# Performance work log

Hardware: AMD Instinct MI355X
Metric: run time of the kernel (lower is better)

The kernel has to match this reference:

```python
import jax, jax.numpy as jnp
import numpy as np

N = 50000      # num_nodes
SEQ = 52       # seq_len (weeks)
FIN = 16       # in_channels
H = 128        # hidden_dim
E = 800000     # num edges (before self-loops)
NEG_SLOPE = 0.2


def setup_inputs() -> dict:
    key = jax.random.key(0)
    ks = jax.random.split(key, 10)
    return {
        "x_seq": jax.random.normal(ks[0], (SEQ, N, FIN), jnp.float32),
        "edge_index": jax.random.randint(ks[1], (2, E), 0, N),
        "Wg": jax.random.normal(ks[2], (FIN, H), jnp.float32) * 0.1,       # GAT linear (no bias on lin in PyG default path; bias added at end)
        "att_src": jax.random.normal(ks[3], (H,), jnp.float32) * 0.1,
        "att_dst": jax.random.normal(ks[4], (H,), jnp.float32) * 0.1,
        "bias_g": jnp.zeros((H,), jnp.float32),
        "W_ih": jax.random.normal(ks[5], (3 * H, H), jnp.float32) * 0.05,  # GRUCell input weights (r,z,n order)
        "W_hh": jax.random.normal(ks[6], (3 * H, H), jnp.float32) * 0.05,
        "b_ih": jnp.zeros((3 * H,), jnp.float32),
        "b_hh": jnp.zeros((3 * H,), jnp.float32),
        "W_fc": jax.random.normal(ks[7], (1, H), jnp.float32) * 0.1,
        "b_fc": jnp.zeros((1,), jnp.float32),
    }


def _gat(x, src, dst, Wg, att_src, att_dst, bias_g):
    # x: [N, FIN] -> xp: [N, H]
    xp = x @ Wg
    a_s = xp @ att_src  # [N]
    a_d = xp @ att_dst  # [N]
    e = jax.nn.leaky_relu(a_s[src] + a_d[dst], NEG_SLOPE)          # [E+N] edge scores
    m = jax.ops.segment_max(e, dst, num_segments=N)                # softmax over incoming edges per dst
    w = jnp.exp(e - m[dst])
    denom = jax.ops.segment_sum(w, dst, num_segments=N)
    alpha = w / denom[dst]
    out = jax.ops.segment_sum(alpha[:, None] * xp[src], dst, num_segments=N)  # [N, H]
    return out + bias_g


def _gru_cell(x, h, W_ih, W_hh, b_ih, b_hh):
    gi = x @ W_ih.T + b_ih  # [N, 3H]
    gh = h @ W_hh.T + b_hh
    i_r, i_z, i_n = jnp.split(gi, 3, axis=1)
    h_r, h_z, h_n = jnp.split(gh, 3, axis=1)
    r = jax.nn.sigmoid(i_r + h_r)
    z = jax.nn.sigmoid(i_z + h_z)
    n = jnp.tanh(i_n + r * h_n)
    return (1.0 - z) * n + z * h


def reference(x_seq, edge_index, Wg, att_src, att_dst, bias_g, W_ih, W_hh, b_ih, b_hh, W_fc, b_fc):
    # PyG GATConv add_self_loops=True
    loop = jnp.arange(N)
    src = jnp.concatenate([edge_index[0], loop])
    dst = jnp.concatenate([edge_index[1], loop])

    def step(h, xt):
        spatial = jax.nn.relu(_gat(xt, src, dst, Wg, att_src, att_dst, bias_g))
        h_new = _gru_cell(spatial, h, W_ih, W_hh, b_ih, b_hh)
        return h_new, None

    h0 = jnp.zeros((N, H), jnp.float32)
    hT, _ = jax.lax.scan(step, h0, x_seq)
    return hT @ W_fc.T + b_fc  # [N, 1]
```

## Files before the change

kernel.cpp:

```cpp
#include <hip/hip_runtime.h>
#include <math.h>

#define NN 50000
#define SEQ 52
#define FIN 16
#define HD 128
#define NEG_SLOPE 0.2f

typedef short bf16x8 __attribute__((ext_vector_type(8)));
typedef float f32x16 __attribute__((ext_vector_type(16)));

__device__ __forceinline__ short f2bf(float x) {
    unsigned u = __float_as_uint(x);
    u += 0x7fffu + ((u >> 16) & 1u);
    return (short)(u >> 16);
}
__device__ __forceinline__ float b2f(short s) {
    return __uint_as_float(((unsigned)(unsigned short)s) << 16);
}

__global__ void deg_init_kernel(int* deg, int n) {
    int i = blockIdx.x * blockDim.x + threadIdx.x;
    if (i < n) deg[i] = 1;
}

__global__ void deg_count_kernel(const int* __restrict__ dst, int* deg, int e) {
    int i = blockIdx.x * blockDim.x + threadIdx.x;
    if (i < e) atomicAdd(&deg[dst[i]], 1);
}

__global__ __launch_bounds__(1024) void scan_kernel(const int* __restrict__ deg,
                                                    int* row_ptr, int n) {
    __shared__ int buf[1024];
    __shared__ int carry;
    int tid = threadIdx.x;
    if (tid == 0) carry = 0;
    __syncthreads();
    for (int base = 0; base < n; base += 1024) {
        int i = base + tid;
        int v = (i < n) ? deg[i] : 0;
        buf[tid] = v;
        __syncthreads();
        for (int off = 1; off < 1024; off <<= 1) {
            int t = (tid >= off) ? buf[tid - off] : 0;
            __syncthreads();
            buf[tid] += t;
            __syncthreads();
        }
        if (i < n) row_ptr[i] = carry + buf[tid] - v;
        __syncthreads();
        if (tid == 1023) carry += buf[1023];
        __syncthreads();
    }
    if (tid == 0) row_ptr[n] = carry;
}

__global__ void selfloop_kernel(const int* __restrict__ row_ptr, int* cursor,
                                int* col, int n) {
    int i = blockIdx.x * blockDim.x + threadIdx.x;
    if (i < n) {
        int p = row_ptr[i];
        col[p] = i;
        cursor[i] = p + 1;
    }
}

__global__ void scatter_kernel(const int* __restrict__ src, const int* __restrict__ dst,
                               int* cursor, int* col, int e) {
    int i = blockIdx.x * blockDim.x + threadIdx.x;
    if (i < e) {
        int p = atomicAdd(&cursor[dst[i]], 1);
        col[p] = src[i];
    }
}

__global__ void wpack_kernel(const float* __restrict__ Wi, const float* __restrict__ Wh,
                             short* __restrict__ wfrag) {
    int idx = blockIdx.x * blockDim.x + threadIdx.x;
    if (idx >= 3 * 4 * 8 * 4 * 64) return;
    int lane = idx & 63;
    int which = (idx >> 6) & 3;
    int ks = (idx >> 8) & 7;
    int slab = (idx >> 11) & 3;
    int g = idx >> 13;
    int col = slab * 32 + (lane & 31);
    int kcol = ks * 16 + (lane >> 5) * 8;
    const float* Wsrc = (which < 2) ? Wi : Wh;
    const float* row = Wsrc + (size_t)(g * HD + col) * HD + kcol;
    short* dstp = wfrag + (size_t)idx * 8;
    bool lo = (which & 1);
#pragma unroll
    for (int e = 0; e < 8; ++e) {
        float v = row[e];
        short hi = f2bf(v);
        dstp[e] = lo ? f2bf(v - b2f(hi)) : hi;
    }
}


__global__ __launch_bounds__(256) void xp_kernel(
    const float* __restrict__ x, const float* __restrict__ Wg,
    const float* __restrict__ att_src, const float* __restrict__ att_dst,
    unsigned* __restrict__ xpb, float* __restrict__ a_s, float* __restrict__ a_d, int n) {
    int wave = (blockIdx.x * blockDim.x + threadIdx.x) >> 6;
    int lane = threadIdx.x & 63;
    if (wave >= n) return;
    const float* xr = x + (size_t)wave * FIN;
    float xv[FIN];
#pragma unroll
    for (int k = 0; k < FIN; ++k) xv[k] = xr[k];
    int c0 = 2 * lane, c1 = 2 * lane + 1;
    float v0 = 0.f, v1 = 0.f;
#pragma unroll
    for (int k = 0; k < FIN; ++k) {
        v0 += xv[k] * Wg[k * HD + c0];
        v1 += xv[k] * Wg[k * HD + c1];
    }
    unsigned p = (unsigned)(unsigned short)f2bf(v0) |
                 ((unsigned)(unsigned short)f2bf(v1) << 16);
    xpb[(size_t)wave * 64 + lane] = p;
    float s = v0 * att_src[c0] + v1 * att_src[c1];
    float d = v0 * att_dst[c0] + v1 * att_dst[c1];
#pragma unroll
    for (int off = 32; off; off >>= 1) {
        s += __shfl_xor(s, off);
        d += __shfl_xor(d, off);
    }
    if (lane == 0) { a_s[wave] = s; a_d[wave] = d; }
}

__global__ __launch_bounds__(256) void gat_kernel(
    const int* __restrict__ row_ptr, const int* __restrict__ col,
    const float* __restrict__ a_s, const float* __restrict__ a_d,
    const short* __restrict__ xpb, const float* __restrict__ bias_g,
    float* __restrict__ spatial, int n) {
    int wave = (blockIdx.x * blockDim.x + threadIdx.x) >> 6;
    int lane = threadIdx.x & 63;
    if (wave >= n) return;
    int start = row_ptr[wave], end = row_ptr[wave + 1];
    int eg = lane >> 4;
    int fg = lane & 15;
    float ad = a_d[wave];
    float acc[8] = {0.f, 0.f, 0.f, 0.f, 0.f, 0.f, 0.f, 0.f};
    float dpart = 0.f;

    for (int base = start; base < end; base += 64) {
        int cnt = end - base;
        if (cnt > 64) cnt = 64;

        int s = 0;
        float wgt = 0.f;
        if (lane < cnt) {
            s = col[base + lane];
            float e = a_s[s] + ad;
            e = (e > 0.f) ? e : NEG_SLOPE * e;
            wgt = __expf(e);
        }
        dpart += wgt;

        int nk = (cnt + 3) >> 2;
        int k = 0;
        for (; k + 2 <= nk; k += 2) {
            int e0 = eg + 4 * k;
            int e1 = e0 + 4;
            int c0 = (e0 < cnt) ? e0 : 0;
            int c1 = (e1 < cnt) ? e1 : 0;
            int si0 = __shfl(s, c0);
            int si1 = __shfl(s, c1);
            float w0 = __shfl(wgt, c0);
            float w1 = __shfl(wgt, c1);
            if (e0 >= cnt) w0 = 0.f;
            if (e1 >= cnt) w1 = 0.f;
            bf16x8 r0 = *(const bf16x8*)(xpb + (size_t)si0 * HD + fg * 8);
            bf16x8 r1 = *(const bf16x8*)(xpb + (size_t)si1 * HD + fg * 8);
#pragma unroll
            for (int j = 0; j < 8; ++j) acc[j] += w0 * b2f(r0[j]);
#pragma unroll
            for (int j = 0; j < 8; ++j) acc[j] += w1 * b2f(r1[j]);
        }
        if (k < nk) {
            int e0 = eg + 4 * k;
            int c0 = (e0 < cnt) ? e0 : 0;
            int si0 = __shfl(s, c0);
            float w0 = __shfl(wgt, c0);
            if (e0 >= cnt) w0 = 0.f;
            bf16x8 r0 = *(const bf16x8*)(xpb + (size_t)si0 * HD + fg * 8);
#pragma unroll
            for (int j = 0; j < 8; ++j) acc[j] += w0 * b2f(r0[j]);
        }
    }

#pragma unroll
    for (int off = 32; off; off >>= 1) dpart += __shfl_xor(dpart, off);
#pragma unroll
    for (int j = 0; j < 8; ++j) {
        acc[j] += __shfl_xor(acc[j], 16);
        acc[j] += __shfl_xor(acc[j], 32);
    }
    float inv = 1.f / dpart;
#pragma unroll
    for (int jj = 0; jj < 2; ++jj) {
        int f = fg * 8 + eg * 2 + jj;
        float o = acc[eg * 2 + jj] * inv + bias_g[f];
        spatial[(size_t)wave * HD + f] = fmaxf(o, 0.f);
    }
}

__global__ __launch_bounds__(256, 2) void gru_mfma_kernel(
    const float* __restrict__ spatial, float* __restrict__ h,
    const short* __restrict__ wfrag,
    const float* __restrict__ b_ih, const float* __restrict__ b_hh, int n) {
    __shared__ bf16x8 sSH[512];
    __shared__ bf16x8 sSL[512];
    __shared__ bf16x8 sHH[512];
    __shared__ bf16x8 sHL[512];

    int t = threadIdx.x;
    int lane = t & 63;
    int w = t >> 6;
    int n0 = blockIdx.x * 32;

#pragma unroll
    for (int q = 0; q < 2; ++q) {
        int ks = w * 2 + q;
        int row = n0 + (lane & 31);
        if (row >= n) row = n - 1;
        int kcol = ks * 16 + (lane >> 5) * 8;
        const float* sp = spatial + (size_t)row * HD + kcol;
        const float* hp = h + (size_t)row * HD + kcol;
        float s8[8], h8[8];
        *(float4*)(s8) = *(const float4*)(sp);
        *(float4*)(s8 + 4) = *(const float4*)(sp + 4);
        *(float4*)(h8) = *(const float4*)(hp);
        *(float4*)(h8 + 4) = *(const float4*)(hp + 4);
        bf16x8 sh, sl, hh, hl;
#pragma unroll
        for (int j = 0; j < 8; ++j) {
            short a = f2bf(s8[j]);
            sh[j] = a;
            sl[j] = f2bf(s8[j] - b2f(a));
            short b = f2bf(h8[j]);
            hh[j] = b;
            hl[j] = f2bf(h8[j] - b2f(b));
        }
        int li = ks * 64 + lane;
        sSH[li] = sh; sSL[li] = sl; sHH[li] = hh; sHL[li] = hl;
    }
    __syncthreads();

    int j0 = w * 32;
    int cj = lane & 31;
    int kh = lane >> 5;

    f32x16 arz[2], ain, ahn;
#pragma unroll
    for (int r = 0; r < 16; ++r) {
        arz[0][r] = 0.f; arz[1][r] = 0.f; ain[r] = 0.f; ahn[r] = 0.f;
    }

    const short* wb = wfrag + (size_t)w * 16384 + (size_t)lane * 8;

    bf16x8 wv[3][12];
#pragma unroll
    for (int p = 0; p < 2; ++p) {
#pragma unroll
        for (int g = 0; g < 3; ++g) {
#pragma unroll
            for (int q = 0; q < 4; ++q)
                wv[p][g * 4 + q] = *(const bf16x8*)(wb + g * 65536 + p * 2048 + q * 512);
        }
    }

#pragma unroll
    for (int ks = 0; ks < 8; ++ks) {
        int cur = ks % 3;
        if (ks < 6) {
            int nxt = (ks + 2) % 3;
#pragma unroll
            for (int g = 0; g < 3; ++g) {
#pragma unroll
                for (int q = 0; q < 4; ++q)
                    wv[nxt][g * 4 + q] =
                        *(const bf16x8*)(wb + g * 65536 + (ks + 2) * 2048 + q * 512);
            }
        }
        int li = ks * 64 + lane;
        bf16x8 aSH = sSH[li];
        bf16x8 aSL = sSL[li];
        bf16x8 aHH = sHH[li];
        bf16x8 aHL = sHL[li];
#pragma unroll
        for (int g = 0; g < 2; ++g) {
            bf16x8 wih = wv[cur][g * 4 + 0];
            bf16x8 wil = wv[cur][g * 4 + 1];
            bf16x8 whh = wv[cur][g * 4 + 2];
            bf16x8 whl = wv[cur][g * 4 + 3];
            arz[g] = __builtin_amdgcn_mfma_f32_32x32x16_bf16(aSH, wih, arz[g], 0, 0, 0);
            arz[g] = __builtin_amdgcn_mfma_f32_32x32x16_bf16(aHH, whh, arz[g], 0, 0, 0);
            arz[g] = __builtin_amdgcn_mfma_f32_32x32x16_bf16(aSL, wih, arz[g], 0, 0, 0);
            arz[g] = __builtin_amdgcn_mfma_f32_32x32x16_bf16(aHL, whh, arz[g], 0, 0, 0);
            arz[g] = __builtin_amdgcn_mfma_f32_32x32x16_bf16(aSH, wil, arz[g], 0, 0, 0);
            arz[g] = __builtin_amdgcn_mfma_f32_32x32x16_bf16(aHH, whl, arz[g], 0, 0, 0);
        }
        {
            bf16x8 wih = wv[cur][8];
            bf16x8 wil = wv[cur][9];
            bf16x8 whh = wv[cur][10];
            bf16x8 whl = wv[cur][11];
            ain = __builtin_amdgcn_mfma_f32_32x32x16_bf16(aSH, wih, ain, 0, 0, 0);
            ahn = __builtin_amdgcn_mfma_f32_32x32x16_bf16(aHH, whh, ahn, 0, 0, 0);
            ain = __builtin_amdgcn_mfma_f32_32x32x16_bf16(aSL, wih, ain, 0, 0, 0);
            ahn = __builtin_amdgcn_mfma_f32_32x32x16_bf16(aHL, whh, ahn, 0, 0, 0);
            ain = __builtin_amdgcn_mfma_f32_32x32x16_bf16(aSH, wil, ain, 0, 0, 0);
            ahn = __builtin_amdgcn_mfma_f32_32x32x16_bf16(aHH, whl, ahn, 0, 0, 0);
        }
    }

    int j = j0 + cj;
    float brz0 = b_ih[j] + b_hh[j];
    float brz1 = b_ih[HD + j] + b_hh[HD + j];
    float bin_ = b_ih[2 * HD + j];
    float bhn = b_hh[2 * HD + j];
    const short* hhs = (const short*)sHH;
    const short* hls = (const short*)sHL;
    int ksj = j >> 4, halfj = (j >> 3) & 1, ej = j & 7;

#pragma unroll
    for (int r = 0; r < 16; ++r) {
        int nl = (r & 3) + 8 * (r >> 2) + 4 * kh;
        int node = n0 + nl;
        if (node < n) {
            float rr = 1.f / (1.f + __expf(-(arz[0][r] + brz0)));
            float zz = 1.f / (1.f + __expf(-(arz[1][r] + brz1)));
            float nn2 = tanhf(ain[r] + bin_ + rr * (ahn[r] + bhn));
            int li = (ksj * 64 + nl + 32 * halfj) * 8 + ej;
            float hold = b2f(hhs[li]) + b2f(hls[li]);
            h[(size_t)node * HD + j] = (1.f - zz) * nn2 + zz * hold;
        }
    }
}

__global__ __launch_bounds__(256) void fc_kernel(
    const float* __restrict__ h, const float* __restrict__ W_fc,
    const float* __restrict__ b_fc, float* __restrict__ out, int n) {
    int wave = (blockIdx.x * blockDim.x + threadIdx.x) >> 6;
    int lane = threadIdx.x & 63;
    if (wave >= n) return;
    float v = h[(size_t)wave * HD + lane] * W_fc[lane] +
              h[(size_t)wave * HD + lane + 64] * W_fc[lane + 64];
#pragma unroll
    for (int off = 32; off; off >>= 1) v += __shfl_xor(v, off);
    if (lane == 0) out[wave] = v + b_fc[0];
}

extern "C" void kernel_launch(void* const* d_in, const int* in_sizes, int n_in,
                              void* d_out, int out_size, void* d_ws, size_t ws_size,
                              hipStream_t stream) {
    const float* x_seq   = (const float*)d_in[0];
    const int*   ei      = (const int*)d_in[1];
    const float* Wg      = (const float*)d_in[2];
    const float* att_src = (const float*)d_in[3];
    const float* att_dst = (const float*)d_in[4];
    const float* bias_g  = (const float*)d_in[5];
    const float* W_ih    = (const float*)d_in[6];
    const float* W_hh    = (const float*)d_in[7];
    const float* b_ih    = (const float*)d_in[8];
    const float* b_hh    = (const float*)d_in[9];
    const float* W_fc    = (const float*)d_in[10];
    const float* b_fc    = (const float*)d_in[11];
    float* out = (float*)d_out;

    const int N = NN;
    const int E = in_sizes[1] / 2;
    const int* src = ei;
    const int* dst = ei + E;

    char* w = (char*)d_ws;
    size_t off = 0;
    auto alloc = [&](size_t bytes) {
        char* p = w + off;
        off = (off + bytes + 255) & ~(size_t)255;
        return p;
    };
    int*   deg     = (int*)alloc((size_t)N * 4);
    int*   row_ptr = (int*)alloc((size_t)(N + 1) * 4);
    int*   cursor  = (int*)alloc((size_t)N * 4);
    int*   col     = (int*)alloc((size_t)(E + N) * 4);
    float* a_s     = (float*)alloc((size_t)N * 4);
    float* a_d     = (float*)alloc((size_t)N * 4);
    unsigned* xpb  = (unsigned*)alloc((size_t)N * 64 * 4);
    float* spatial = (float*)alloc((size_t)N * HD * 4);
    float* hbuf    = (float*)alloc((size_t)N * HD * 4);
    short* wfrag   = (short*)alloc((size_t)3 * 4 * 8 * 4 * 64 * 8 * 2);

    hipMemsetAsync(hbuf, 0, (size_t)N * HD * 4, stream);

    deg_init_kernel<<<(N + 255) / 256, 256, 0, stream>>>(deg, N);
    deg_count_kernel<<<(E + 255) / 256, 256, 0, stream>>>(dst, deg, E);
    scan_kernel<<<1, 1024, 0, stream>>>(deg, row_ptr, N);
    selfloop_kernel<<<(N + 255) / 256, 256, 0, stream>>>(row_ptr, cursor, col, N);
    scatter_kernel<<<(E + 255) / 256, 256, 0, stream>>>(src, dst, cursor, col, E);
    wpack_kernel<<<(24576 + 255) / 256, 256, 0, stream>>>(W_ih, W_hh, wfrag);

    int node_wave_blocks = (N * 64 + 255) / 256;
    int gru_blocks = (N + 31) / 32;

    for (int t = 0; t < SEQ; ++t) {
        const float* xt = x_seq + (size_t)t * N * FIN;
        xp_kernel<<<node_wave_blocks, 256, 0, stream>>>(xt, Wg, att_src, att_dst,
                                                        xpb, a_s, a_d, N);
        gat_kernel<<<node_wave_blocks, 256, 0, stream>>>(row_ptr, col, a_s, a_d,
                                                         (const short*)xpb, bias_g,
                                                         spatial, N);
        gru_mfma_kernel<<<gru_blocks, 256, 0, stream>>>(spatial, hbuf, wfrag,
                                                        b_ih, b_hh, N);
    }
    fc_kernel<<<node_wave_blocks, 256, 0, stream>>>(hbuf, W_fc, b_fc, out, N);
}
```

Measured before the change: 6.574 ms.

## Process two node tiles per GRU block and unroll GAT gather by four

The GRU MFMA kernel now covers 64 nodes per block in two 32-row tiles, so each loaded weight fragment feeds both tiles. This halves the weight traffic per node, but it drops the register prefetch pipeline for weights and doubles the accumulators and shared memory. The GAT aggregation loop is unrolled to four edges per iteration so more gather loads are in flight at once. Division, sigmoid and tanh are replaced by fast __fdividef/__expf forms, which trade a little accuracy for fewer instructions.

```diff
diff --git a/kernel.cpp b/kernel.cpp
--- a/kernel.cpp
+++ b/kernel.cpp
@@ -160,25 +160,27 @@
 
         int nk = (cnt + 3) >> 2;
         int k = 0;
-        for (; k + 2 <= nk; k += 2) {
-            int e0 = eg + 4 * k;
-            int e1 = e0 + 4;
-            int c0 = (e0 < cnt) ? e0 : 0;
-            int c1 = (e1 < cnt) ? e1 : 0;
-            int si0 = __shfl(s, c0);
-            int si1 = __shfl(s, c1);
-            float w0 = __shfl(wgt, c0);
-            float w1 = __shfl(wgt, c1);
-            if (e0 >= cnt) w0 = 0.f;
-            if (e1 >= cnt) w1 = 0.f;
-            bf16x8 r0 = *(const bf16x8*)(xpb + (size_t)si0 * HD + fg * 8);
-            bf16x8 r1 = *(const bf16x8*)(xpb + (size_t)si1 * HD + fg * 8);
-#pragma unroll
-            for (int j = 0; j < 8; ++j) acc[j] += w0 * b2f(r0[j]);
-#pragma unroll
-            for (int j = 0; j < 8; ++j) acc[j] += w1 * b2f(r1[j]);
-        }
-        if (k < nk) {
+        for (; k + 4 <= nk; k += 4) {
+            int si[4];
+            float wt[4];
+#pragma unroll
+            for (int u = 0; u < 4; ++u) {
+                int e0 = eg + 4 * (k + u);
+                int c0 = (e0 < cnt) ? e0 : 0;
+                si[u] = __shfl(s, c0);
+                wt[u] = __shfl(wgt, c0);
+                if (e0 >= cnt) wt[u] = 0.f;
+            }
+            bf16x8 r[4];
+#pragma unroll
+            for (int u = 0; u < 4; ++u)
+                r[u] = *(const bf16x8*)(xpb + (size_t)si[u] * HD + fg * 8);
+#pragma unroll
+            for (int u = 0; u < 4; ++u)
+#pragma unroll
+                for (int j = 0; j < 8; ++j) acc[j] += wt[u] * b2f(r[u][j]);
+        }
+        for (; k < nk; ++k) {
             int e0 = eg + 4 * k;
             int c0 = (e0 < cnt) ? e0 : 0;
             int si0 = __shfl(s, c0);
@@ -197,7 +199,7 @@
         acc[j] += __shfl_xor(acc[j], 16);
         acc[j] += __shfl_xor(acc[j], 32);
     }
-    float inv = 1.f / dpart;
+    float inv = __fdividef(1.f, dpart);
 #pragma unroll
     for (int jj = 0; jj < 2; ++jj) {
         int f = fg * 8 + eg * 2 + jj;
@@ -210,20 +212,21 @@
     const float* __restrict__ spatial, float* __restrict__ h,
     const short* __restrict__ wfrag,
     const float* __restrict__ b_ih, const float* __restrict__ b_hh, int n) {
-    __shared__ bf16x8 sSH[512];
-    __shared__ bf16x8 sSL[512];
-    __shared__ bf16x8 sHH[512];
-    __shared__ bf16x8 sHL[512];
+    __shared__ bf16x8 sSH[2][512];
+    __shared__ bf16x8 sSL[2][512];
+    __shared__ bf16x8 sHH[2][512];
+    __shared__ bf16x8 sHL[2][512];
 
     int t = threadIdx.x;
     int lane = t & 63;
     int w = t >> 6;
-    int n0 = blockIdx.x * 32;
-
-#pragma unroll
-    for (int q = 0; q < 2; ++q) {
-        int ks = w * 2 + q;
-        int row = n0 + (lane & 31);
+    int n0 = blockIdx.x * 64;
+
+#pragma unroll
+    for (int q = 0; q < 4; ++q) {
+        int tile = q >> 1;
+        int ks = w * 2 + (q & 1);
+        int row = n0 + tile * 32 + (lane & 31);
         if (row >= n) row = n - 1;
         int kcol = ks * 16 + (lane >> 5) * 8;
         const float* sp = spatial + (size_t)row * HD + kcol;
@@ -244,7 +247,8 @@
             hl[j] = f2bf(h8[j] - b2f(b));
         }
         int li = ks * 64 + lane;
-        sSH[li] = sh; sSL[li] = sl; sHH[li] = hh; sHL[li] = hl;
+        sSH[tile][li] = sh; sSL[tile][li] = sl;
+        sHH[tile][li] = hh; sHL[tile][li] = hl;
     }
     __syncthreads();
 
@@ -252,67 +256,58 @@
     int cj = lane & 31;
     int kh = lane >> 5;
 
-    f32x16 arz[2], ain, ahn;
-#pragma unroll
-    for (int r = 0; r < 16; ++r) {
-        arz[0][r] = 0.f; arz[1][r] = 0.f; ain[r] = 0.f; ahn[r] = 0.f;
-    }
+    f32x16 arz[2][2], ain[2], ahn[2];
+#pragma unroll
+    for (int tile = 0; tile < 2; ++tile)
+#pragma unroll
+        for (int r = 0; r < 16; ++r) {
+            arz[tile][0][r] = 0.f; arz[tile][1][r] = 0.f;
+            ain[tile][r] = 0.f; ahn[tile][r] = 0.f;
+        }
 
     const short* wb = wfrag + (size_t)w * 16384 + (size_t)lane * 8;
 
-    bf16x8 wv[3][12];
-#pragma unroll
-    for (int p = 0; p < 2; ++p) {
-#pragma unroll
-        for (int g = 0; g < 3; ++g) {
+#pragma unroll
+    for (int ks = 0; ks < 8; ++ks) {
+        bf16x8 wv[12];
+#pragma unroll
+        for (int g = 0; g < 3; ++g)
 #pragma unroll
             for (int q = 0; q < 4; ++q)
-                wv[p][g * 4 + q] = *(const bf16x8*)(wb + g * 65536 + p * 2048 + q * 512);
-        }
-    }
-
-#pragma unroll
-    for (int ks = 0; ks < 8; ++ks) {
-        int cur = ks % 3;
-        if (ks < 6) {
-            int nxt = (ks + 2) % 3;
-#pragma unroll
-            for (int g = 0; g < 3; ++g) {
-#pragma unroll
-                for (int q = 0; q < 4; ++q)
-                    wv[nxt][g * 4 + q] =
-                        *(const bf16x8*)(wb + g * 65536 + (ks + 2) * 2048 + q * 512);
+                wv[g * 4 + q] = *(const bf16x8*)(wb + g * 65536 + ks * 2048 + q * 512);
+
+        int li = ks * 64 + lane;
+#pragma unroll
+        for (int tile = 0; tile < 2; ++tile) {
+            bf16x8 aSH = sSH[tile][li];
+            bf16x8 aSL = sSL[tile][li];
+            bf16x8 aHH = sHH[tile][li];
+            bf16x8 aHL = sHL[tile][li];
+#pragma unroll
+            for (int g = 0; g < 2; ++g) {
+                bf16x8 wih = wv[g * 4 + 0];
+                bf16x8 wil = wv[g * 4 + 1];
+                bf16x8 whh = wv[g * 4 + 2];
+                bf16x8 whl = wv[g * 4 + 3];
+                arz[tile][g] = __builtin_amdgcn_mfma_f32_32x32x16_bf16(aSH, wih, arz[tile][g], 0, 0, 0);
+                arz[tile][g] = __builtin_amdgcn_mfma_f32_32x32x16_bf16(aHH, whh, arz[tile][g], 0, 0, 0);
+                arz[tile][g] = __builtin_amdgcn_mfma_f32_32x32x16_bf16(aSL, wih, arz[tile][g], 0, 0, 0);
+                arz[tile][g] = __builtin_amdgcn_mfma_f32_32x32x16_bf16(aHL, whh, arz[tile][g], 0, 0, 0);
+                arz[tile][g] = __builtin_amdgcn_mfma_f32_32x32x16_bf16(aSH, wil, arz[tile][g], 0, 0, 0);
+                arz[tile][g] = __builtin_amdgcn_mfma_f32_32x32x16_bf16(aHH, whl, arz[tile][g], 0, 0, 0);
             }
-        }
-        int li = ks * 64 + lane;
-        bf16x8 aSH = sSH[li];
-        bf16x8 aSL = sSL[li];
-        bf16x8 aHH = sHH[li];
-        bf16x8 aHL = sHL[li];
-#pragma unroll
-        for (int g = 0; g < 2; ++g) {
-            bf16x8 wih = wv[cur][g * 4 + 0];
-            bf16x8 wil = wv[cur][g * 4 + 1];
-            bf16x8 whh = wv[cur][g * 4 + 2];
-            bf16x8 whl = wv[cur][g * 4 + 3];
-            arz[g] = __builtin_amdgcn_mfma_f32_32x32x16_bf16(aSH, wih, arz[g], 0, 0, 0);
-            arz[g] = __builtin_amdgcn_mfma_f32_32x32x16_bf16(aHH, whh, arz[g], 0, 0, 0);
-            arz[g] = __builtin_amdgcn_mfma_f32_32x32x16_bf16(aSL, wih, arz[g], 0, 0, 0);
-            arz[g] = __builtin_amdgcn_mfma_f32_32x32x16_bf16(aHL, whh, arz[g], 0, 0, 0);
-            arz[g] = __builtin_amdgcn_mfma_f32_32x32x16_bf16(aSH, wil, arz[g], 0, 0, 0);
-            arz[g] = __builtin_amdgcn_mfma_f32_32x32x16_bf16(aHH, whl, arz[g], 0, 0, 0);
-        }
-        {
-            bf16x8 wih = wv[cur][8];
-            bf16x8 wil = wv[cur][9];
-            bf16x8 whh = wv[cur][10];
-            bf16x8 whl = wv[cur][11];
-            ain = __builtin_amdgcn_mfma_f32_32x32x16_bf16(aSH, wih, ain, 0, 0, 0);
-            ahn = __builtin_amdgcn_mfma_f32_32x32x16_bf16(aHH, whh, ahn, 0, 0, 0);
-            ain = __builtin_amdgcn_mfma_f32_32x32x16_bf16(aSL, wih, ain, 0, 0, 0);
-            ahn = __builtin_amdgcn_mfma_f32_32x32x16_bf16(aHL, whh, ahn, 0, 0, 0);
-            ain = __builtin_amdgcn_mfma_f32_32x32x16_bf16(aSH, wil, ain, 0, 0, 0);
-            ahn = __builtin_amdgcn_mfma_f32_32x32x16_bf16(aHH, whl, ahn, 0, 0, 0);
+            {
+                bf16x8 wih = wv[8];
+                bf16x8 wil = wv[9];
+                bf16x8 whh = wv[10];
+                bf16x8 whl = wv[11];
+                ain[tile] = __builtin_amdgcn_mfma_f32_32x32x16_bf16(aSH, wih, ain[tile], 0, 0, 0);
+                ahn[tile] = __builtin_amdgcn_mfma_f32_32x32x16_bf16(aHH, whh, ahn[tile], 0, 0, 0);
+                ain[tile] = __builtin_amdgcn_mfma_f32_32x32x16_bf16(aSL, wih, ain[tile], 0, 0, 0);
+                ahn[tile] = __builtin_amdgcn_mfma_f32_32x32x16_bf16(aHL, whh, ahn[tile], 0, 0, 0);
+                ain[tile] = __builtin_amdgcn_mfma_f32_32x32x16_bf16(aSH, wil, ain[tile], 0, 0, 0);
+                ahn[tile] = __builtin_amdgcn_mfma_f32_32x32x16_bf16(aHH, whl, ahn[tile], 0, 0, 0);
+            }
         }
     }
 
@@ -321,21 +316,26 @@
     float brz1 = b_ih[HD + j] + b_hh[HD + j];
     float bin_ = b_ih[2 * HD + j];
     float bhn = b_hh[2 * HD + j];
-    const short* hhs = (const short*)sHH;
-    const short* hls = (const short*)sHL;
     int ksj = j >> 4, halfj = (j >> 3) & 1, ej = j & 7;
 
 #pragma unroll
-    for (int r = 0; r < 16; ++r) {
-        int nl = (r & 3) + 8 * (r >> 2) + 4 * kh;
-        int node = n0 + nl;
-        if (node < n) {
-            float rr = 1.f / (1.f + __expf(-(arz[0][r] + brz0)));
-            float zz = 1.f / (1.f + __expf(-(arz[1][r] + brz1)));
-            float nn2 = tanhf(ain[r] + bin_ + rr * (ahn[r] + bhn));
-            int li = (ksj * 64 + nl + 32 * halfj) * 8 + ej;
-            float hold = b2f(hhs[li]) + b2f(hls[li]);
-            h[(size_t)node * HD + j] = (1.f - zz) * nn2 + zz * hold;
+    for (int tile = 0; tile < 2; ++tile) {
+        const short* hhs = (const short*)&sHH[tile][0];
+        const short* hls = (const short*)&sHL[tile][0];
+#pragma unroll
+        for (int r = 0; r < 16; ++r) {
+            int nl = (r & 3) + 8 * (r >> 2) + 4 * kh;
+            int node = n0 + tile * 32 + nl;
+            if (node < n) {
+                float rr = __fdividef(1.f, 1.f + __expf(-(arz[tile][0][r] + brz0)));
+                float zz = __fdividef(1.f, 1.f + __expf(-(arz[tile][1][r] + brz1)));
+                float u = ain[tile][r] + bin_ + rr * (ahn[tile][r] + bhn);
+                float ex = __expf(2.f * u);
+                float nn2 = 1.f - __fdividef(2.f, ex + 1.f);
+                int li = (ksj * 64 + nl + 32 * halfj) * 8 + ej;
+                float hold = b2f(hhs[li]) + b2f(hls[li]);
+                h[(size_t)node * HD + j] = (1.f - zz) * nn2 + zz * hold;
+            }
         }
     }
 }
@@ -403,7 +403,7 @@
     wpack_kernel<<<(24576 + 255) / 256, 256, 0, stream>>>(W_ih, W_hh, wfrag);
 
     int node_wave_blocks = (N * 64 + 255) / 256;
-    int gru_blocks = (N + 31) / 32;
+    int gru_blocks = (N + 63) / 64;
 
     for (int t = 0; t < SEQ; ++t) {
         const float* xt = x_seq + (size_t)t * N * FIN;
```

Result: slower. 6.772 ms (+3.0%).
